# Optimization experiments

Hardware: AMD Instinct MI355X
Metric: run time of the kernel (lower is better)

Reference implementation:

```python
import jax, jax.numpy as jnp
import numpy as np

EMBED_DIM = 1024
NUM_HEADS = 16
HEAD_DIM = EMBED_DIM // NUM_HEADS
SCALE = HEAD_DIM ** -0.5


def setup_inputs() -> dict:
    key = jax.random.key(0)
    k1, k2, k3, k4, k5, k6 = jax.random.split(key, 6)
    B, Tq, Tk = 2, 2048, 2048
    std = EMBED_DIM ** -0.5
    return {
        "x_q": jax.random.normal(k1, (B, Tq, EMBED_DIM), jnp.float32),
        "x_kv": jax.random.normal(k2, (B, Tk, EMBED_DIM), jnp.float32),
        "w_q": jax.random.normal(k3, (EMBED_DIM, EMBED_DIM), jnp.float32) * std,
        "w_kv": jax.random.normal(k4, (EMBED_DIM, 2 * EMBED_DIM), jnp.float32) * std,
        "w_proj": jax.random.normal(k5, (EMBED_DIM, EMBED_DIM), jnp.float32) * std,
        "w_rel": jax.random.normal(k6, (1, NUM_HEADS), jnp.float32) * 0.02,
    }


def reference(x_q, x_kv, w_q, w_kv, w_proj, w_rel):
    B, Tq, _ = x_q.shape
    Tk = x_kv.shape[1]
    # projections
    q = x_q @ w_q                       # [B,Tq,E]
    kv = x_kv @ w_kv                    # [B,Tk,2E]
    k, v = jnp.split(kv, 2, axis=-1)

    def heads(y, T):
        return y.reshape(B, T, NUM_HEADS, HEAD_DIM).transpose(0, 2, 1, 3)

    q = heads(q, Tq)                    # [B,H,Tq,D]
    k = heads(k, Tk)
    v = heads(v, Tk)

    logits = jnp.einsum('bhqd,bhkd->bhqk', q, k) * SCALE  # [B,H,Tq,Tk]

    # relative position bias: Dense(1 -> H) applied to (pos_q - pos_k)
    rel = jnp.arange(Tq, dtype=jnp.float32)[:, None] - jnp.arange(Tk, dtype=jnp.float32)[None, :]
    bias = rel[..., None] * w_rel[0]                      # [Tq,Tk,H]
    bias = bias.transpose(2, 0, 1)[None]                  # [1,H,Tq,Tk]
    logits = logits + bias

    attn = jax.nn.softmax(logits, axis=-1)                # dropout=0 / inference -> identity
    out = jnp.einsum('bhqk,bhkd->bhqd', attn, v)          # [B,H,Tq,D]
    out = out.transpose(0, 2, 1, 3).reshape(B, Tq, EMBED_DIM)
    return out @ w_proj
```

## Files before the change

kernel.cpp:

```cpp
#include <hip/hip_runtime.h>
#include <hip/hip_bf16.h>

typedef __attribute__((ext_vector_type(8))) short short8;
typedef __attribute__((ext_vector_type(8))) __bf16 bf16x8;
typedef __attribute__((ext_vector_type(4))) float f32x4;
typedef __attribute__((ext_vector_type(8))) unsigned short ushort8v;
typedef __attribute__((ext_vector_type(4))) unsigned short ushort4v;

#define NB 2
#define TQ 2048
#define TKK 2048
#define EMB 1024
#define NH 16
#define HD 64

__device__ __forceinline__ unsigned short f2bf(float f){
  union { float f; unsigned u; } v; v.f = f;
  unsigned r = v.u + 0x7FFFu + ((v.u >> 16) & 1u);
  return (unsigned short)(r >> 16);
}

#define GLOAD_LDS16(g, l) __builtin_amdgcn_global_load_lds( \
    (const __attribute__((address_space(1))) void*)(g), \
    (__attribute__((address_space(3))) void*)(l), 16, 0, 0)

#define SWZ(row, inner) ((inner) ^ (((row)&7)<<4))

__device__ __forceinline__ void mfma16(const short8& a, const short8& b, f32x4& c){
  c = __builtin_amdgcn_mfma_f32_16x16x32_bf16(
        __builtin_bit_cast(bf16x8, a), __builtin_bit_cast(bf16x8, b), c, 0, 0, 0);
}

__device__ __forceinline__ void cvt_body(const float* __restrict__ in,
    unsigned short* __restrict__ out, int i){
  float4 v = ((const float4*)in)[i];
  ushort4v o;
  o.x = f2bf(v.x); o.y = f2bf(v.y); o.z = f2bf(v.z); o.w = f2bf(v.w);
  ((ushort4v*)out)[i] = o;
}

__device__ __forceinline__ void wt_body(const float* __restrict__ W,
    unsigned short* __restrict__ WT, int K, int N, int k0, int n0,
    unsigned short (*tile)[72]){
  int tid = threadIdx.x;
  #pragma unroll
  for (int it=0; it<4; ++it){
    int c = tid + it*256;
    int r = c>>4, c4 = (c&15)*4;
    float4 v = *(const float4*)(W + (long)(k0+r)*N + n0 + c4);
    tile[r][c4+0]=f2bf(v.x); tile[r][c4+1]=f2bf(v.y);
    tile[r][c4+2]=f2bf(v.z); tile[r][c4+3]=f2bf(v.w);
  }
  __syncthreads();
  #pragma unroll
  for (int it=0; it<2; ++it){
    int c = tid + it*256;
    int n = c>>3, k8 = (c&7)*8;
    ushort8v o;
    #pragma unroll
    for (int j=0;j<8;++j) o[j] = tile[k8+j][n];
    *(ushort8v*)(WT + (long)(n0+n)*K + k0 + k8) = o;
  }
}

__global__ __launch_bounds__(256) void prep_kernel(
    const float* __restrict__ x_q, const float* __restrict__ x_kv,
    const float* __restrict__ w_q, const float* __restrict__ w_kv,
    const float* __restrict__ w_proj,
    unsigned short* __restrict__ Aq,  unsigned short* __restrict__ Akv,
    unsigned short* __restrict__ WqT, unsigned short* __restrict__ WkvT,
    unsigned short* __restrict__ WpT){
  __shared__ unsigned short tile[64][72];
  const int bx = blockIdx.x;
  if (bx < 4096){
    cvt_body(x_q, Aq, bx*256 + threadIdx.x);
  } else if (bx < 8192){
    cvt_body(x_kv, Akv, (bx-4096)*256 + threadIdx.x);
  } else if (bx < 8448){
    int blk = bx - 8192;
    wt_body(w_q, WqT, EMB, EMB, (blk>>4)*64, (blk&15)*64, tile);
  } else if (bx < 8960){
    int blk = bx - 8448;
    wt_body(w_kv, WkvT, EMB, 2*EMB, (blk>>5)*64, (blk&31)*64, tile);
  } else {
    int blk = bx - 8960;
    wt_body(w_proj, WpT, EMB, EMB, (blk>>4)*64, (blk&15)*64, tile);
  }
}

template<int MODE>
__device__ __forceinline__ void gemm_body(const unsigned short* __restrict__ A,
    const unsigned short* __restrict__ BT, void* __restrict__ Cout,
    int M, int N, int K, int m0, int n0,
    unsigned short* Al, unsigned short* Bl){
  const int tid = threadIdx.x;
  const int wave = tid>>6, lane = tid&63;
  const int wm = (wave>>1)*64, wn = (wave&1)*64;
  const int g = lane>>4, lr = lane&15;
  const int srow = lane>>3;
  const int sinner = (lane&7)*16;
  f32x4 acc[4][4] = {};

  for (int k0=0; k0<K; k0+=64){
    #pragma unroll
    for (int j=0;j<4;++j){
      int chunk = wave*4 + j;
      int row = chunk*8 + srow;
      int kb = SWZ(row, sinner);
      GLOAD_LDS16(A + (long)(m0+row)*K + k0 + (kb>>1), Al + chunk*512);
      GLOAD_LDS16(BT + (long)(n0+row)*K + k0 + (kb>>1), Bl + chunk*512);
    }
    __syncthreads();
    #pragma unroll
    for (int kk=0;kk<2;++kk){
      short8 af[4], bfr[4];
      const int kbyte = kk*64 + g*16;
      #pragma unroll
      for (int i=0;i<4;++i){
        int ar = wm + i*16 + lr;
        af[i] = *(const short8*)((const char*)Al + ar*128 + SWZ(ar, kbyte));
        int br = wn + i*16 + lr;
        bfr[i] = *(const short8*)((const char*)Bl + br*128 + SWZ(br, kbyte));
      }
      #pragma unroll
      for (int i=0;i<4;++i)
        #pragma unroll
        for (int jn=0;jn<4;++jn)
          mfma16(af[i], bfr[jn], acc[i][jn]);
    }
    __syncthreads();
  }
  #pragma unroll
  for (int i=0;i<4;++i){
    int row = m0 + wm + i*16 + g*4;
    #pragma unroll
    for (int jn=0;jn<4;++jn){
      if (MODE == 2){
        int dg = n0 - EMB + wn + jn*16 + lr;
        int h = dg >> 6, d = dg & 63;
        int b = row >> 11, t = row & (TKK-1);
        ushort4v w;
        #pragma unroll
        for (int r=0;r<4;++r) w[r] = f2bf(acc[i][jn][r]);
        *(ushort4v*)((unsigned short*)Cout + ((long)((b*NH + h)*HD + d)*TKK + t)) = w;
      } else {
        int col = n0 + wn + jn*16 + lr;
        #pragma unroll
        for (int r=0;r<4;++r){
          if (MODE == 1)
            ((unsigned short*)Cout)[(long)(row+r)*N + col] = f2bf(acc[i][jn][r]);
          else
            ((float*)Cout)[(long)(row+r)*N + col] = acc[i][jn][r];
        }
      }
    }
  }
}

__global__ __launch_bounds__(256,3) void gemm_qkv(
    const unsigned short* __restrict__ Aq,  const unsigned short* __restrict__ WqT,  unsigned short* __restrict__ Qb,
    const unsigned short* __restrict__ Akv, const unsigned short* __restrict__ WkvT,
    unsigned short* __restrict__ Kb, unsigned short* __restrict__ VT){
  __shared__ unsigned short Al[128*64];
  __shared__ unsigned short Bl[128*64];
  const int x = blockIdx.x;
  if (x < 8)
    gemm_body<1>(Aq,  WqT,  Qb, NB*TQ, EMB, EMB, blockIdx.y*128, x*128, Al, Bl);
  else if (x < 16)
    gemm_body<1>(Akv, WkvT, Kb, NB*TKK, EMB, EMB, blockIdx.y*128, (x-8)*128, Al, Bl);
  else
    gemm_body<2>(Akv, WkvT, VT, NB*TKK, EMB, EMB, blockIdx.y*128, EMB + (x-16)*128, Al, Bl);
}

__global__ __launch_bounds__(256,2) void gemm_out(const unsigned short* __restrict__ A,
    const unsigned short* __restrict__ BT, float* __restrict__ C,
    int M, int N, int K){
  __shared__ unsigned short Al[64*64];
  __shared__ unsigned short Bl[128*64];
  const int tid = threadIdx.x;
  const int wave = tid>>6, lane = tid&63;
  const int m0 = blockIdx.y*64, n0 = blockIdx.x*128;
  const int wm = (wave>>1)*32, wn = (wave&1)*64;
  const int g = lane>>4, lr = lane&15;
  const int srow = lane>>3;
  const int sinner = (lane&7)*16;
  f32x4 acc[2][4] = {};

  for (int k0=0; k0<K; k0+=64){
    #pragma unroll
    for (int j=0;j<2;++j){
      int chunk = wave*2 + j;
      int row = chunk*8 + srow;
      int kb = SWZ(row, sinner);
      GLOAD_LDS16(A + (long)(m0+row)*K + k0 + (kb>>1), Al + chunk*512);
    }
    #pragma unroll
    for (int j=0;j<4;++j){
      int chunk = wave*4 + j;
      int row = chunk*8 + srow;
      int kb = SWZ(row, sinner);
      GLOAD_LDS16(BT + (long)(n0+row)*K + k0 + (kb>>1), Bl + chunk*512);
    }
    __syncthreads();
    #pragma unroll
    for (int kk=0;kk<2;++kk){
      short8 af[2], bfr[4];
      const int kbyte = kk*64 + g*16;
      #pragma unroll
      for (int i=0;i<2;++i){
        int ar = wm + i*16 + lr;
        af[i] = *(const short8*)((const char*)Al + ar*128 + SWZ(ar, kbyte));
      }
      #pragma unroll
      for (int jn=0;jn<4;++jn){
        int br = wn + jn*16 + lr;
        bfr[jn] = *(const short8*)((const char*)Bl + br*128 + SWZ(br, kbyte));
      }
      #pragma unroll
      for (int i=0;i<2;++i)
        #pragma unroll
        for (int jn=0;jn<4;++jn)
          mfma16(af[i], bfr[jn], acc[i][jn]);
    }
    __syncthreads();
  }
  #pragma unroll
  for (int i=0;i<2;++i){
    int row = m0 + wm + i*16 + g*4;
    #pragma unroll
    for (int jn=0;jn<4;++jn){
      int col = n0 + wn + jn*16 + lr;
      #pragma unroll
      for (int r=0;r<4;++r)
        C[(long)(row+r)*N + col] = acc[i][jn][r];
    }
  }
}

__global__ __launch_bounds__(512,4) void attn_kernel(const unsigned short* __restrict__ Qb,
    const unsigned short* __restrict__ Kb, const unsigned short* __restrict__ VT,
    const float* __restrict__ w_rel, unsigned short* __restrict__ Ob){
  __shared__ unsigned short Kl[3][64*64];
  __shared__ unsigned short Vl[3][64*64];
  __shared__ __attribute__((aligned(16))) char Pl[8][16*128];
  const int id  = blockIdx.x + 16*blockIdx.y;
  const int nid = (id & 7)*64 + (id >> 3);
  const int qb  = nid & 15, bh = nid >> 4;
  const int b = bh>>4, h = bh&15;
  const int q0 = qb*128;
  const int tid = threadIdx.x, wave = tid>>6, lane = tid&63;
  const int g = lane>>4, lr = lane&15;
  const int srow = lane>>3, sinner = (lane&7)*16;
  const float C1 = 0.125f*1.44269504f;
  const float wr2 = w_rel[h]*1.44269504f;
  const float w64 = 64.0f*wr2;
  char* Pw = &Pl[wave][0];

  const int strow = wave*8 + srow;
  const int skb = SWZ(strow, sinner);
  const unsigned short* Kg = Kb + (long)(b*TKK + strow)*EMB + h*HD + (skb>>1);
  const unsigned short* Vg = VT + (long)(bh*HD + strow)*TKK + (skb>>1);

  short8 qf[2];
  #pragma unroll
  for (int kk=0;kk<2;++kk)
    qf[kk] = *(const short8*)(Qb + (long)(b*TQ + q0 + wave*16 + lr)*EMB + h*HD + kk*32 + g*8);

  const float bq = (float)(q0 + wave*16 + lr)*wr2;
  float dq[4][4];
  #pragma unroll
  for (int n=0;n<4;++n)
    #pragma unroll
    for (int r=0;r<4;++r)
      dq[n][r] = bq - (float)(n*16 + 4*g + r)*wr2;

  short8 ones;
  #pragma unroll
  for (int j=0;j<8;++j) ones[j] = (short)0x3F80;

  f32x4 oacc[4] = {};
  f32x4 lacc = {};
  float Mxs = -1e30f;

  GLOAD_LDS16(Kg, &Kl[0][wave*512]);
  GLOAD_LDS16(Vg, &Vl[0][wave*512]);
  GLOAD_LDS16(Kg + (long)64*EMB, &Kl[1][wave*512]);
  GLOAD_LDS16(Vg + 64, &Vl[1][wave*512]);
  asm volatile("s_waitcnt vmcnt(2)" ::: "memory");
  __builtin_amdgcn_s_barrier();

  int cur = 0;
  for (int kt=0; kt<TKK; kt+=64){
    const bool issue = (kt + 128 < TKK);
    int nxt2 = cur + 2; if (nxt2 >= 3) nxt2 -= 3;
    if (issue){
      GLOAD_LDS16(Kg + (long)(kt+128)*EMB, &Kl[nxt2][wave*512]);
      GLOAD_LDS16(Vg + (kt+128), &Vl[nxt2][wave*512]);
    }

    f32x4 sacc[4] = {};
    __builtin_amdgcn_s_setprio(1);
    #pragma unroll
    for (int kk=0;kk<2;++kk){
      short8 kf[4];
      const int kbyte = kk*64 + g*16;
      #pragma unroll
      for (int n=0;n<4;++n){
        int trow = n*16 + lr;
        kf[n] = *(const short8*)((const char*)&Kl[cur][0] + trow*128 + SWZ(trow, kbyte));
      }
      #pragma unroll
      for (int n=0;n<4;++n)
        mfma16(kf[n], qf[kk], sacc[n]);
    }
    __builtin_amdgcn_s_setprio(0);

    #pragma unroll
    for (int n=0;n<4;++n)
      #pragma unroll
      for (int r=0;r<4;++r)
        sacc[n][r] = fmaf(sacc[n][r], C1, dq[n][r]);

    float rowmax;
    {
      float m0 = fmaxf(fmaxf(sacc[0][0],sacc[0][1]),sacc[0][2]);
      float m1 = fmaxf(fmaxf(sacc[0][3],sacc[1][0]),sacc[1][1]);
      float m2 = fmaxf(fmaxf(sacc[1][2],sacc[1][3]),sacc[2][0]);
      float m3 = fmaxf(fmaxf(sacc[2][1],sacc[2][2]),sacc[2][3]);
      float m4 = fmaxf(fmaxf(sacc[3][0],sacc[3][1]),sacc[3][2]);
      float a  = fmaxf(fmaxf(m0,m1),m2);
      float bb = fmaxf(fmaxf(m3,m4),sacc[3][3]);
      rowmax = fmaxf(a,bb);
      rowmax = fmaxf(rowmax, __shfl_xor(rowmax, 16, 64));
      rowmax = fmaxf(rowmax, __shfl_xor(rowmax, 32, 64));
    }

    if (__any(rowmax > Mxs + 8.0f)){
      float Mn = fmaxf(Mxs, rowmax);
      float rf = exp2f(Mxs - Mn);
      Mxs = Mn;
      float rfo[4];
      #pragma unroll
      for (int r=0;r<4;++r) rfo[r] = __shfl(rf, 4*g + r, 64);
      #pragma unroll
      for (int n=0;n<4;++n)
        #pragma unroll
        for (int r=0;r<4;++r) oacc[n][r] *= rfo[r];
      #pragma unroll
      for (int r=0;r<4;++r) lacc[r] *= rfo[r];
    }

    #pragma unroll
    for (int n=0;n<4;++n){
      ushort4v w;
      #pragma unroll
      for (int r=0;r<4;++r)
        w[r] = __builtin_bit_cast(unsigned short, __float2bfloat16(exp2f(sacc[n][r]-Mxs)));
      *(ushort4v*)(Pw + lr*128 + SWZ(lr, 32*n + 8*g)) = w;
    }

    asm volatile("" ::: "memory");

    __builtin_amdgcn_s_setprio(1);
    #pragma unroll
    for (int kk=0;kk<2;++kk){
      const int kbyte = kk*64 + g*16;
      short8 pf = *(const short8*)(Pw + lr*128 + SWZ(lr, kbyte));
      #pragma unroll
      for (int n=0;n<4;++n){
        int vrow = n*16 + lr;
        short8 vf = *(const short8*)((const char*)&Vl[cur][0] + vrow*128 + SWZ(vrow, kbyte));
        mfma16(pf, vf, oacc[n]);
      }
      mfma16(pf, ones, lacc);
    }
    __builtin_amdgcn_s_setprio(0);

    Mxs += w64;

    if (issue) asm volatile("s_waitcnt vmcnt(2) lgkmcnt(0)" ::: "memory");
    else       asm volatile("s_waitcnt vmcnt(0) lgkmcnt(0)" ::: "memory");
    __builtin_amdgcn_s_barrier();
    cur += 1; if (cur >= 3) cur -= 3;
  }

  #pragma unroll
  for (int r=0;r<4;++r){
    float inv = 1.0f / lacc[r];
    int q = q0 + wave*16 + 4*g + r;
    #pragma unroll
    for (int n=0;n<4;++n){
      int d = n*16 + lr;
      Ob[(long)(b*TQ + q)*EMB + h*HD + d] = f2bf(oacc[n][r]*inv);
    }
  }
}

extern "C" void kernel_launch(void* const* d_in, const int* in_sizes, int n_in,
                              void* d_out, int out_size, void* d_ws, size_t ws_size,
                              hipStream_t stream){
  const float* x_q    = (const float*)d_in[0];
  const float* x_kv   = (const float*)d_in[1];
  const float* w_q    = (const float*)d_in[2];
  const float* w_kv   = (const float*)d_in[3];
  const float* w_proj = (const float*)d_in[4];
  const float* w_rel  = (const float*)d_in[5];
  (void)in_sizes; (void)n_in; (void)out_size; (void)ws_size;
  char* ws = (char*)d_ws;
  const size_t MB = 1024*1024;
  unsigned short* Qb   = (unsigned short*)(ws + 0);
  unsigned short* Kb   = (unsigned short*)(ws + 8*MB);
  unsigned short* VT   = (unsigned short*)(ws + 16*MB);
  unsigned short* WpT  = (unsigned short*)(ws + 24*MB);
  unsigned short* WqT  = (unsigned short*)(ws + 26*MB);
  unsigned short* WkvT = (unsigned short*)(ws + 28*MB);
  unsigned short* Aq   = (unsigned short*)(ws + 32*MB);
  unsigned short* Akv  = (unsigned short*)(ws + 40*MB);
  unsigned short* Ob   = Aq;
  float* out = (float*)d_out;

  prep_kernel<<<9216, 256, 0, stream>>>(x_q, x_kv, w_q, w_kv, w_proj,
                                        Aq, Akv, WqT, WkvT, WpT);
  gemm_qkv<<<dim3(24,32), 256, 0, stream>>>(Aq, WqT, Qb, Akv, WkvT, Kb, VT);
  attn_kernel<<<dim3(16,32), 512, 0, stream>>>(Qb, Kb, VT, w_rel, Ob);
  gemm_out<<<dim3(8,64), 256, 0, stream>>>(Ob, WpT, out, NB*TQ, EMB, EMB);
}
```

Measured before the change: 144.9 us.

## Fold relative-position bias into V scaling and denominator fragment, remap QKV GEMM blocks

```diff
diff --git a/kernel.cpp b/kernel.cpp
--- a/kernel.cpp
+++ b/kernel.cpp
@@ -92,7 +92,7 @@
 __device__ __forceinline__ void gemm_body(const unsigned short* __restrict__ A,
     const unsigned short* __restrict__ BT, void* __restrict__ Cout,
     int M, int N, int K, int m0, int n0,
-    unsigned short* Al, unsigned short* Bl){
+    unsigned short* Al, unsigned short* Bl, const float* __restrict__ w_rel){
   const int tid = threadIdx.x;
   const int wave = tid>>6, lane = tid&63;
   const int wm = (wave>>1)*64, wn = (wave&1)*64;
@@ -139,9 +139,12 @@
         int dg = n0 - EMB + wn + jn*16 + lr;
         int h = dg >> 6, d = dg & 63;
         int b = row >> 11, t = row & (TKK-1);
+        float wr2h = w_rel[h]*1.44269504f;
+        float fac = exp2f(-(float)(t & 63)*wr2h);
+        float stp = exp2f(-wr2h);
         ushort4v w;
         #pragma unroll
-        for (int r=0;r<4;++r) w[r] = f2bf(acc[i][jn][r]);
+        for (int r=0;r<4;++r){ w[r] = f2bf(acc[i][jn][r]*fac); fac *= stp; }
         *(ushort4v*)((unsigned short*)Cout + ((long)((b*NH + h)*HD + d)*TKK + t)) = w;
       } else {
         int col = n0 + wn + jn*16 + lr;
@@ -160,16 +163,19 @@
 __global__ __launch_bounds__(256,3) void gemm_qkv(
     const unsigned short* __restrict__ Aq,  const unsigned short* __restrict__ WqT,  unsigned short* __restrict__ Qb,
     const unsigned short* __restrict__ Akv, const unsigned short* __restrict__ WkvT,
-    unsigned short* __restrict__ Kb, unsigned short* __restrict__ VT){
+    unsigned short* __restrict__ Kb, unsigned short* __restrict__ VT,
+    const float* __restrict__ w_rel){
   __shared__ unsigned short Al[128*64];
   __shared__ unsigned short Bl[128*64];
-  const int x = blockIdx.x;
+  const int p = blockIdx.x + 24*blockIdx.y;
+  const int x = (p & 7) + 8*((p >> 3) % 3);
+  const int y = (p >> 3) / 3;
   if (x < 8)
-    gemm_body<1>(Aq,  WqT,  Qb, NB*TQ, EMB, EMB, blockIdx.y*128, x*128, Al, Bl);
+    gemm_body<1>(Aq,  WqT,  Qb, NB*TQ, EMB, EMB, y*128, x*128, Al, Bl, nullptr);
   else if (x < 16)
-    gemm_body<1>(Akv, WkvT, Kb, NB*TKK, EMB, EMB, blockIdx.y*128, (x-8)*128, Al, Bl);
+    gemm_body<1>(Akv, WkvT, Kb, NB*TKK, EMB, EMB, y*128, (x-8)*128, Al, Bl, nullptr);
   else
-    gemm_body<2>(Akv, WkvT, VT, NB*TKK, EMB, EMB, blockIdx.y*128, EMB + (x-16)*128, Al, Bl);
+    gemm_body<2>(Akv, WkvT, VT, NB*TKK, EMB, EMB, y*128, EMB + (x-16)*128, Al, Bl, w_rel);
 }
 
 __global__ __launch_bounds__(256,2) void gemm_out(const unsigned short* __restrict__ A,
@@ -266,17 +272,12 @@
   for (int kk=0;kk<2;++kk)
     qf[kk] = *(const short8*)(Qb + (long)(b*TQ + q0 + wave*16 + lr)*EMB + h*HD + kk*32 + g*8);
 
-  const float bq = (float)(q0 + wave*16 + lr)*wr2;
-  float dq[4][4];
-  #pragma unroll
-  for (int n=0;n<4;++n)
-    #pragma unroll
-    for (int r=0;r<4;++r)
-      dq[n][r] = bq - (float)(n*16 + 4*g + r)*wr2;
-
-  short8 ones;
-  #pragma unroll
-  for (int j=0;j<8;++j) ones[j] = (short)0x3F80;
+  short8 cfrag[2];
+  #pragma unroll
+  for (int kk=0;kk<2;++kk)
+    #pragma unroll
+    for (int j=0;j<8;++j)
+      cfrag[kk][j] = (short)f2bf(exp2f(-(float)(kk*32 + g*8 + j)*wr2));
 
   f32x4 oacc[4] = {};
   f32x4 lacc = {};
@@ -314,12 +315,6 @@
         mfma16(kf[n], qf[kk], sacc[n]);
     }
     __builtin_amdgcn_s_setprio(0);
-
-    #pragma unroll
-    for (int n=0;n<4;++n)
-      #pragma unroll
-      for (int r=0;r<4;++r)
-        sacc[n][r] = fmaf(sacc[n][r], C1, dq[n][r]);
 
     float rowmax;
     {
@@ -334,9 +329,10 @@
       rowmax = fmaxf(rowmax, __shfl_xor(rowmax, 16, 64));
       rowmax = fmaxf(rowmax, __shfl_xor(rowmax, 32, 64));
     }
-
-    if (__any(rowmax > Mxs + 8.0f)){
-      float Mn = fmaxf(Mxs, rowmax);
+    float rowmax_s = rowmax*C1;
+
+    if (__any(rowmax_s > Mxs + 8.0f)){
+      float Mn = fmaxf(Mxs, rowmax_s);
       float rf = exp2f(Mxs - Mn);
       Mxs = Mn;
       float rfo[4];
@@ -355,7 +351,8 @@
       ushort4v w;
       #pragma unroll
       for (int r=0;r<4;++r)
-        w[r] = __builtin_bit_cast(unsigned short, __float2bfloat16(exp2f(sacc[n][r]-Mxs)));
+        w[r] = __builtin_bit_cast(unsigned short,
+                 __float2bfloat16(exp2f(fmaf(sacc[n][r], C1, -Mxs))));
       *(ushort4v*)(Pw + lr*128 + SWZ(lr, 32*n + 8*g)) = w;
     }
 
@@ -372,7 +369,7 @@
         short8 vf = *(const short8*)((const char*)&Vl[cur][0] + vrow*128 + SWZ(vrow, kbyte));
         mfma16(pf, vf, oacc[n]);
       }
-      mfma16(pf, ones, lacc);
+      mfma16(pf, cfrag[kk], lacc);
     }
     __builtin_amdgcn_s_setprio(0);
 
@@ -421,7 +418,7 @@
 
   prep_kernel<<<9216, 256, 0, stream>>>(x_q, x_kv, w_q, w_kv, w_proj,
                                         Aq, Akv, WqT, WkvT, WpT);
-  gemm_qkv<<<dim3(24,32), 256, 0, stream>>>(Aq, WqT, Qb, Akv, WkvT, Kb, VT);
+  gemm_qkv<<<dim3(24,32), 256, 0, stream>>>(Aq, WqT, Qb, Akv, WkvT, Kb, VT, w_rel);
   attn_kernel<<<dim3(16,32), 512, 0, stream>>>(Qb, Kb, VT, w_rel, Ob);
   gemm_out<<<dim3(8,64), 256, 0, stream>>>(Ob, WpT, out, NB*TQ, EMB, EMB);
 }
```

New measurement: 144.6 us. About the same (-0.2%).
